# Performance work log

Measured on AMD Instinct MI355X. Metric: run time of the kernel, lower is better.

## Reference

```python
import jax, jax.numpy as jnp
import numpy as np

K = 20
CH_IN = [6, 128, 128, 256]
CH_OUT = [64, 64, 128, 256]
EMB = 1024


def _knn_idx(x, k):
    # x: (B, C, N) -> (B, N, k) indices of k nearest neighbors (incl. self)
    inner = jnp.einsum('bcn,bcm->bnm', x, x)
    xx = jnp.sum(x * x, axis=1)  # (B, N)
    pd = 2.0 * inner - xx[:, :, None] - xx[:, None, :]  # = -||xi - xj||^2
    return jax.lax.top_k(pd, k)[1]


def _graph_feature(x, k):
    # x: (B, C, N) -> (B, 2C, N, k) EdgeConv features [x_j - x_i, x_i]
    xt = jnp.transpose(x, (0, 2, 1))  # (B, N, C)
    idx = _knn_idx(x, k)  # (B, N, k)
    nb = jax.vmap(lambda f, i: f[i])(xt, idx)  # (B, N, k, C) gather
    center = xt[:, :, None, :]
    feat = jnp.concatenate([nb - center, jnp.broadcast_to(center, nb.shape)], axis=-1)
    return jnp.transpose(feat, (0, 3, 1, 2))  # (B, 2C, N, k)


def _bn(y, g, b, m, v):
    # eval-mode BatchNorm over channel axis 1 (or last for 2D input is also axis 1)
    shp = (1, -1) + (1,) * (y.ndim - 2)
    s = g / jnp.sqrt(v + 1e-5)
    return (y - m.reshape(shp)) * s.reshape(shp) + b.reshape(shp)


def setup_inputs() -> dict:
    key = jax.random.key(0)
    ks = iter(jax.random.split(key, 64))
    rn = lambda shape: jax.random.normal(next(ks), shape, jnp.float32) * 0.05
    ru = lambda shape: jax.random.uniform(next(ks), shape, jnp.float32, minval=0.5, maxval=1.5)
    d = {"x": jax.random.normal(next(ks), (16, 1024, 3), jnp.float32)}
    for i, (ci, co) in enumerate(zip(CH_IN, CH_OUT)):
        d[f"c{i}_w"] = rn((co, ci)); d[f"c{i}_b"] = rn((co,))
        d[f"c{i}_g"] = ru((co,)); d[f"c{i}_be"] = rn((co,))
        d[f"c{i}_m"] = rn((co,)); d[f"c{i}_v"] = ru((co,))
    cat = sum(CH_OUT)  # 512
    d["lc_w"] = rn((EMB, cat)); d["lc_b"] = rn((EMB,))
    d["lc_g"] = ru((EMB,)); d["lc_be"] = rn((EMB,))
    d["lc_m"] = rn((EMB,)); d["lc_v"] = ru((EMB,))
    d["l0_w"] = rn((512, 2 * EMB))
    d["l0_g"] = ru((512,)); d["l0_be"] = rn((512,)); d["l0_m"] = rn((512,)); d["l0_v"] = ru((512,))
    d["l1_w"] = rn((256, 512)); d["l1_b"] = rn((256,))
    d["l1_g"] = ru((256,)); d["l1_be"] = rn((256,)); d["l1_m"] = rn((256,)); d["l1_v"] = ru((256,))
    d["ow"] = rn((40, 256)); d["ob"] = rn((40,))
    return d


def reference(x, c0_w, c0_b, c0_g, c0_be, c0_m, c0_v,
              c1_w, c1_b, c1_g, c1_be, c1_m, c1_v,
              c2_w, c2_b, c2_g, c2_be, c2_m, c2_v,
              c3_w, c3_b, c3_g, c3_be, c3_m, c3_v,
              lc_w, lc_b, lc_g, lc_be, lc_m, lc_v,
              l0_w, l0_g, l0_be, l0_m, l0_v,
              l1_w, l1_b, l1_g, l1_be, l1_m, l1_v,
              ow, ob):
    convs = [(c0_w, c0_b, c0_g, c0_be, c0_m, c0_v),
             (c1_w, c1_b, c1_g, c1_be, c1_m, c1_v),
             (c2_w, c2_b, c2_g, c2_be, c2_m, c2_v),
             (c3_w, c3_b, c3_g, c3_be, c3_m, c3_v)]
    cur = jnp.transpose(x, (0, 2, 1))  # (B, 3, N)
    outs = []
    for w, b, g, be, m, v in convs:
        f = _graph_feature(cur, K)  # (B, 2C_in, N, k)
        y = jnp.einsum('bcnk,oc->bonk', f, w) + b[None, :, None, None]  # 1x1 conv2d
        y = jax.nn.leaky_relu(_bn(y, g, be, m, v), 0.2)
        cur = jnp.max(y, axis=-1)  # max over k neighbors -> (B, C_out, N)
        outs.append(cur)
    h = jnp.concatenate(outs, axis=1)  # (B, 512, N)
    y = jnp.einsum('bcn,oc->bon', h, lc_w) + lc_b[None, :, None]  # 1x1 conv1d
    y = jax.nn.leaky_relu(_bn(y, lc_g, lc_be, lc_m, lc_v), 0.2)  # (B, 1024, N)
    h = jnp.concatenate([jnp.max(y, axis=-1), jnp.mean(y, axis=-1)], axis=1)  # (B, 2048)
    h = jax.nn.leaky_relu(_bn(h @ l0_w.T, l0_g, l0_be, l0_m, l0_v), 0.2)
    h = jax.nn.leaky_relu(_bn(h @ l1_w.T + l1_b, l1_g, l1_be, l1_m, l1_v), 0.2)
    return h @ ow.T + ob  # (B, 40)
```

## Files before the change

### kernel.cpp

```cpp
#include <hip/hip_runtime.h>
#include <hip/hip_bf16.h>

#define BB 16
#define NPTS 1024
#define KNB 20
#define HC 512

__device__ __forceinline__ float XV(const float* __restrict__ X, int b, int n, int c)
{
    return X[((size_t)b * NPTS + n) * 3 + c];
}

__device__ __forceinline__ unsigned long long dist2key(float d, int m)
{
    unsigned u = __float_as_uint(d);
    u = (u & 0x80000000u) ? ~u : (u | 0x80000000u);
    return ((unsigned long long)u << 32) | (unsigned)(1023 - m);
}

__device__ __forceinline__ void wave_topk_write(unsigned long long* key,
                                                int* __restrict__ idxo,
                                                size_t obase, int lane)
{
    for (int it = 0; it < KNB; ++it) {
        unsigned long long best = 0ull; int bj = -1;
#pragma unroll
        for (int j = 0; j < 16; ++j) if (key[j] > best) { best = key[j]; bj = j; }
        unsigned long long wbest = best;
        for (int off = 32; off > 0; off >>= 1) {
            const unsigned long long o = __shfl_down(wbest, off, 64);
            if (o > wbest) wbest = o;
        }
        wbest = __shfl(wbest, 0, 64);
        if (best == wbest && bj >= 0) key[bj] = 0ull;
        if (lane == 0) idxo[obase + it] = 1023 - (int)(wbest & 0xFFFFFFFFull);
    }
}

__global__ void sentinel_kernel(float* __restrict__ out, float val)
{
    const int i = blockIdx.x * 256 + threadIdx.x;
    if (i < BB * 40) out[i] = val;
}

__global__ void xx_kernel(const float* __restrict__ H, const float* __restrict__ X,
                          float* __restrict__ xx, int cin, int off_in, int use_x)
{
    const int p = blockIdx.x * blockDim.x + threadIdx.x;
    if (p >= BB * NPTS) return;
    float s = 0.f;
    if (use_x) {
        const int b = p >> 10, n = p & 1023;
        for (int c = 0; c < 3; ++c) { const float v = XV(X, b, n, c); s += v * v; }
    } else {
        const float4* r4 = (const float4*)(H + (size_t)p * HC + off_in);
        for (int c4 = 0; c4 < cin / 4; ++c4) {
            const float4 v = r4[c4];
            s += v.x*v.x + v.y*v.y + v.z*v.z + v.w*v.w;
        }
    }
    xx[p] = s;
}

template<int CIN>
__global__ __launch_bounds__(256, 3) void knn4_kernel(
    const float* __restrict__ H, const float* __restrict__ xx,
    int* __restrict__ idxo, int off_in)
{
    __shared__ __align__(16) float qv[4][CIN];
    __shared__ float dist[4][NPTS];
    __shared__ float sxxq[4];
    const int blk = blockIdx.x;
    const int q0g = blk * 4;
    const int b = q0g >> 10, q0 = q0g & 1023;
    const int tid = threadIdx.x;
    const int base = b * NPTS;

    for (int t = tid; t < 4 * CIN; t += 256) {
        const int q = t / CIN, c = t - q * CIN;
        qv[q][c] = H[(size_t)(base + q0 + q) * HC + off_in + c];
    }
    if (tid < 4) sxxq[tid] = xx[base + q0 + tid];
    __syncthreads();

    const int g = tid >> 3, l = tid & 7;
    float4 aq[4][CIN / 32];
#pragma unroll
    for (int q = 0; q < 4; ++q)
#pragma unroll
        for (int r = 0; r < CIN / 32; ++r)
            aq[q][r] = *(const float4*)&qv[q][4 * (l + 8 * r)];

    for (int it = 0; it < 32; ++it) {
        const int m = g + 32 * it;
        float acc[4] = {0.f, 0.f, 0.f, 0.f};
#pragma unroll
        for (int r = 0; r < CIN / 32; ++r) {
            const float4 v = *(const float4*)(H + (size_t)(base + m) * HC + off_in + 4 * (l + 8 * r));
#pragma unroll
            for (int q = 0; q < 4; ++q)
                acc[q] += aq[q][r].x*v.x + aq[q][r].y*v.y + aq[q][r].z*v.z + aq[q][r].w*v.w;
        }
#pragma unroll
        for (int q = 0; q < 4; ++q) {
            acc[q] += __shfl_xor(acc[q], 1, 64);
            acc[q] += __shfl_xor(acc[q], 2, 64);
            acc[q] += __shfl_xor(acc[q], 4, 64);
        }
        if (l == 0) {
            const float xxm = xx[base + m];
#pragma unroll
            for (int q = 0; q < 4; ++q)
                dist[q][m] = (2.f * acc[q] - sxxq[q]) - xxm;
        }
    }
    __syncthreads();

    const int w = tid >> 6, lane = tid & 63;
    unsigned long long key[16];
#pragma unroll
    for (int j = 0; j < 16; ++j) {
        const int m = lane + 64 * j;
        key[j] = dist2key(dist[w][m], m);
    }
    wave_topk_write(key, idxo, (size_t)(base + q0 + w) * KNB, lane);
}

__global__ __launch_bounds__(256, 3) void knn4x_kernel(
    const float* __restrict__ X, const float* __restrict__ xx, int* __restrict__ idxo)
{
    __shared__ float qv[4][4];
    __shared__ float dist[4][NPTS];
    __shared__ float sxxq[4];
    const int blk = blockIdx.x;
    const int q0g = blk * 4;
    const int b = q0g >> 10, q0 = q0g & 1023;
    const int tid = threadIdx.x;
    const int base = b * NPTS;

    if (tid < 4) {
        for (int c = 0; c < 3; ++c) qv[tid][c] = XV(X, b, q0 + tid, c);
        sxxq[tid] = xx[base + q0 + tid];
    }
    __syncthreads();

    for (int j = 0; j < 4; ++j) {
        const int m = tid + 256 * j;
        const float r0 = XV(X, b, m, 0), r1 = XV(X, b, m, 1), r2 = XV(X, b, m, 2);
        const float xxm = xx[base + m];
#pragma unroll
        for (int q = 0; q < 4; ++q) {
            const float acc = qv[q][0]*r0 + qv[q][1]*r1 + qv[q][2]*r2;
            dist[q][m] = (2.f * acc - sxxq[q]) - xxm;
        }
    }
    __syncthreads();

    const int w = tid >> 6, lane = tid & 63;
    unsigned long long key[16];
#pragma unroll
    for (int j = 0; j < 16; ++j) {
        const int m = lane + 64 * j;
        key[j] = dist2key(dist[w][m], m);
    }
    wave_topk_write(key, idxo, (size_t)(base + q0 + w) * KNB, lane);
}

__device__ __forceinline__ float wfetch1(const float* __restrict__ W, int og,
                                         int CIN, int COUT, int c)
{
    if (og < COUT) return W[(size_t)og * 2 * CIN + c];
    const float* r0 = W + (size_t)(og - COUT) * 2 * CIN;
    return r0[CIN + c] - r0[c];
}

__global__ __launch_bounds__(256, 4) void gemm_conv_kernel(
    const float* __restrict__ H, const float* __restrict__ W, float* __restrict__ P,
    int off_in, int CIN, int COUT, int NO128)
{
    __shared__ float hl[32][68];
    __shared__ float wl[32][132];
    const int mblk = blockIdx.x / NO128;
    const int oblk = blockIdx.x - mblk * NO128;
    const int tid = threadIdx.x;
    const int o = tid & 63, grp = tid >> 6;
    const int NO = NO128 * 128;
    const int n0 = mblk * 64;
    const int og0 = oblk * 128 + o;
    const int og1 = og0 + 64;

    float acc0[16], acc1[16];
#pragma unroll
    for (int i = 0; i < 16; ++i) { acc0[i] = 0.f; acc1[i] = 0.f; }

    for (int ct = 0; ct < CIN / 32; ++ct) {
        for (int r = 0; r < 2; ++r) {
            const int e = tid + 256 * r;
            const int n = e & 63, c4 = e >> 6;
            const float4 hv = *(const float4*)(H + (size_t)(n0 + n) * HC + off_in + ct * 32 + c4 * 4);
            hl[c4*4+0][n] = hv.x; hl[c4*4+1][n] = hv.y; hl[c4*4+2][n] = hv.z; hl[c4*4+3][n] = hv.w;
        }
        for (int r = 0; r < 16; ++r) {
            const int e = tid + 256 * r;
            const int c_ = e & 31, o_ = e >> 5;
            wl[c_][o_] = wfetch1(W, oblk * 128 + o_, CIN, COUT, ct * 32 + c_);
        }
        __syncthreads();
        for (int c = 0; c < 32; ++c) {
            const float wva = wl[c][o];
            const float wvb = wl[c][o + 64];
            const float* hr = &hl[c][grp * 16];
#pragma unroll
            for (int nn = 0; nn < 4; ++nn) {
                const float4 hv = *(const float4*)(hr + 4 * nn);
                acc0[4*nn+0] += wva * hv.x; acc0[4*nn+1] += wva * hv.y;
                acc0[4*nn+2] += wva * hv.z; acc0[4*nn+3] += wva * hv.w;
                acc1[4*nn+0] += wvb * hv.x; acc1[4*nn+1] += wvb * hv.y;
                acc1[4*nn+2] += wvb * hv.z; acc1[4*nn+3] += wvb * hv.w;
            }
        }
        __syncthreads();
    }

#pragma unroll
    for (int i = 0; i < 16; ++i) {
        P[(size_t)(n0 + grp * 16 + i) * NO + og0] = acc0[i];
        P[(size_t)(n0 + grp * 16 + i) * NO + og1] = acc1[i];
    }
}

template<int COUT>
__global__ __launch_bounds__(COUT) void edge_epi_kernel(
    const float* __restrict__ P, const int* __restrict__ idx,
    const float* __restrict__ Bs, const float* __restrict__ G, const float* __restrict__ Be,
    const float* __restrict__ Bm, const float* __restrict__ Bv,
    float* __restrict__ Hout, int off_out)
{
    constexpr int NO = 2 * COUT;
    const int blk = blockIdx.x;
    const int base = (blk >> 10) << 10;
    const int o = threadIdx.x;
    const float s = G[o] / sqrtf(Bv[o] + 1e-5f);
    const float beo = Be[o];
    const float cb = P[(size_t)blk * NO + COUT + o] + Bs[o] - Bm[o];
    float mx = -INFINITY;
    for (int k = 0; k < KNB; ++k) {
        const int m = idx[(size_t)blk * KNB + k];
        const float v = P[(size_t)(base + m) * NO + o];
        float t = (v + cb) * s + beo;
        t = t > 0.f ? t : 0.2f * t;
        mx = fmaxf(mx, t);
    }
    Hout[(size_t)blk * HC + off_out + o] = mx;
}

template<int CIN, int COUT, bool USEX>
__global__ __launch_bounds__(COUT) void conv_kernel(
    const float* __restrict__ H, const float* __restrict__ X, const int* __restrict__ idx,
    const float* __restrict__ W, const float* __restrict__ Bs, const float* __restrict__ G,
    const float* __restrict__ Be, const float* __restrict__ Bm, const float* __restrict__ Bv,
    float* __restrict__ Hout, int off_in, int off_out)
{
    __shared__ __align__(16) float ctr[CIN];
    __shared__ __align__(16) float nb[KNB][CIN];
    __shared__ int sidx[KNB];
    const int blk = blockIdx.x;
    const int b = blk >> 10, q = blk & 1023;
    const int tid = threadIdx.x;
    const int base = b * NPTS;

    if (tid < KNB) sidx[tid] = idx[(size_t)(base + q) * KNB + tid];
    for (int c = tid; c < CIN; c += COUT)
        ctr[c] = USEX ? XV(X, b, q, c) : H[(size_t)(base + q) * HC + off_in + c];
    __syncthreads();
    for (int t = tid; t < KNB * CIN; t += COUT) {
        const int k = t / CIN, c = t - k * CIN;
        nb[k][c] = USEX ? XV(X, b, sidx[k], c) : H[(size_t)(base + sidx[k]) * HC + off_in + c];
    }
    __syncthreads();

    float acc[KNB];
    float cacc = 0.f;
#pragma unroll
    for (int k = 0; k < KNB; ++k) acc[k] = 0.f;

    const float* wr = W + (size_t)tid * 2 * CIN;
    for (int c = 0; c < CIN; ++c) {
        const float w1 = wr[c], w2 = wr[CIN + c];
        cacc += (w2 - w1) * ctr[c];
#pragma unroll
        for (int k = 0; k < KNB; ++k) acc[k] += w1 * nb[k][c];
    }

    const int o = tid;
    const float s = G[o] / sqrtf(Bv[o] + 1e-5f);
    const float beo = Be[o];
    const float cb = cacc + Bs[o] - Bm[o];
    float mx = -INFINITY;
#pragma unroll
    for (int k = 0; k < KNB; ++k) {
        float t = (acc[k] + cb) * s + beo;
        t = t > 0.f ? t : 0.2f * t;
        mx = fmaxf(mx, t);
    }
    Hout[(size_t)(base + q) * HC + off_out + o] = mx;
}

__global__ __launch_bounds__(256, 4) void lcpool_kernel(
    const float* __restrict__ H, const float* __restrict__ W, const float* __restrict__ Bs,
    const float* __restrict__ G, const float* __restrict__ Be,
    const float* __restrict__ Bm, const float* __restrict__ Bv,
    float* __restrict__ pmax, float* __restrict__ psum)
{
    __shared__ float hl[32][68];
    __shared__ float wl[32][132];
    __shared__ float redm[4][128];
    __shared__ float reds[4][128];
    const int bid = blockIdx.x;
    const int b = bid >> 7;
    const int rem = bid & 127;
    const int oblk = rem >> 4;
    const int nblk = rem & 15;
    const int tid = threadIdx.x;
    const int o = tid & 63;
    const int grp = tid >> 6;
    const int og0 = oblk * 128 + o;
    const int og1 = og0 + 64;
    const int n0 = nblk * 64;
    const size_t hbase = (size_t)b * NPTS * HC;

    float acc0[16], acc1[16];
#pragma unroll
    for (int i = 0; i < 16; ++i) { acc0[i] = 0.f; acc1[i] = 0.f; }

    for (int ct = 0; ct < 16; ++ct) {
        for (int r = 0; r < 2; ++r) {
            const int e = tid + 256 * r;
            const int n = e & 63, c4 = e >> 6;
            const float4 hv = *(const float4*)(H + hbase + (size_t)(n0 + n) * HC + ct * 32 + c4 * 4);
            hl[c4*4+0][n] = hv.x; hl[c4*4+1][n] = hv.y; hl[c4*4+2][n] = hv.z; hl[c4*4+3][n] = hv.w;
        }
        for (int r = 0; r < 16; ++r) {
            const int e = tid + 256 * r;
            const int c_ = e & 31, o_ = e >> 5;
            wl[c_][o_] = W[(size_t)(oblk * 128 + o_) * HC + ct * 32 + c_];
        }
        __syncthreads();
        for (int c = 0; c < 32; ++c) {
            const float wva = wl[c][o];
            const float wvb = wl[c][o + 64];
            const float* hr = &hl[c][grp * 16];
#pragma unroll
            for (int nn = 0; nn < 4; ++nn) {
                const float4 hv = *(const float4*)(hr + 4 * nn);
                acc0[4*nn+0] += wva * hv.x; acc0[4*nn+1] += wva * hv.y;
                acc0[4*nn+2] += wva * hv.z; acc0[4*nn+3] += wva * hv.w;
                acc1[4*nn+0] += wvb * hv.x; acc1[4*nn+1] += wvb * hv.y;
                acc1[4*nn+2] += wvb * hv.z; acc1[4*nn+3] += wvb * hv.w;
            }
        }
        __syncthreads();
    }

#pragma unroll
    for (int p = 0; p < 2; ++p) {
        const int og = p ? og1 : og0;
        const float* acc = p ? acc1 : acc0;
        const float s = G[og] / sqrtf(Bv[og] + 1e-5f);
        const float beo = Be[og];
        const float mb = Bs[og] - Bm[og];
        float pm = -INFINITY, ps = 0.f;
#pragma unroll
        for (int i = 0; i < 16; ++i) {
            float t = (acc[i] + mb) * s + beo;
            t = t > 0.f ? t : 0.2f * t;
            pm = fmaxf(pm, t); ps += t;
        }
        redm[grp][o + 64 * p] = pm; reds[grp][o + 64 * p] = ps;
    }
    __syncthreads();
    if (grp == 0) {
#pragma unroll
        for (int p = 0; p < 2; ++p) {
            const int oo = o + 64 * p;
            float m0 = redm[0][oo], s0 = reds[0][oo];
            for (int i2 = 1; i2 < 4; ++i2) { m0 = fmaxf(m0, redm[i2][oo]); s0 += reds[i2][oo]; }
            pmax[((size_t)b * 16 + nblk) * 1024 + oblk * 128 + oo] = m0;
            psum[((size_t)b * 16 + nblk) * 1024 + oblk * 128 + oo] = s0;
        }
    }
}

__global__ void pool_reduce_kernel(const float* __restrict__ pmax, const float* __restrict__ psum,
                                   float* __restrict__ h2)
{
    const int i = blockIdx.x * 256 + threadIdx.x;
    if (i >= BB * 1024) return;
    const int b = i >> 10, o = i & 1023;
    float mx = -INFINITY, sm = 0.f;
    for (int c = 0; c < 16; ++c) {
        mx = fmaxf(mx, pmax[((size_t)b * 16 + c) * 1024 + o]);
        sm += psum[((size_t)b * 16 + c) * 1024 + o];
    }
    h2[(size_t)b * 2048 + o] = mx;
    h2[(size_t)b * 2048 + 1024 + o] = sm * (1.f / 1024.f);
}

__global__ void l0_kernel(const float* __restrict__ h2, const float* __restrict__ W,
                          const float* __restrict__ G, const float* __restrict__ Be,
                          const float* __restrict__ Bm, const float* __restrict__ Bv,
                          float* __restrict__ h3)
{
    const int i = blockIdx.x * 256 + threadIdx.x;
    if (i >= BB * 512) return;
    const int b = i >> 9, o = i & 511;
    const float4* w4 = (const float4*)(W + (size_t)o * 2048);
    const float4* h4p = (const float4*)(h2 + (size_t)b * 2048);
    float acc = 0.f;
    for (int c = 0; c < 512; ++c) {
        const float4 wv = w4[c]; const float4 hv = h4p[c];
        acc += wv.x*hv.x + wv.y*hv.y + wv.z*hv.z + wv.w*hv.w;
    }
    const float s = G[o] / sqrtf(Bv[o] + 1e-5f);
    float t = (acc - Bm[o]) * s + Be[o];
    t = t > 0.f ? t : 0.2f * t;
    h3[(size_t)b * 512 + o] = t;
}

__global__ void l1_kernel(const float* __restrict__ h3, const float* __restrict__ W,
                          const float* __restrict__ Bs, const float* __restrict__ G,
                          const float* __restrict__ Be, const float* __restrict__ Bm,
                          const float* __restrict__ Bv, float* __restrict__ h4o)
{
    const int i = blockIdx.x * 256 + threadIdx.x;
    if (i >= BB * 256) return;
    const int b = i >> 8, o = i & 255;
    const float4* w4 = (const float4*)(W + (size_t)o * 512);
    const float4* hv4 = (const float4*)(h3 + (size_t)b * 512);
    float acc = 0.f;
    for (int c = 0; c < 128; ++c) {
        const float4 wv = w4[c]; const float4 hv = hv4[c];
        acc += wv.x*hv.x + wv.y*hv.y + wv.z*hv.z + wv.w*hv.w;
    }
    acc += Bs[o];
    const float s = G[o] / sqrtf(Bv[o] + 1e-5f);
    float t = (acc - Bm[o]) * s + Be[o];
    t = t > 0.f ? t : 0.2f * t;
    h4o[(size_t)b * 256 + o] = t;
}

__global__ void out_kernel(const float* __restrict__ h4, const float* __restrict__ W,
                           const float* __restrict__ Bs, float* __restrict__ out)
{
    const int i = blockIdx.x * 256 + threadIdx.x;
    if (i >= BB * 40) return;
    const int b = i / 40, o = i % 40;
    const float4* w4 = (const float4*)(W + (size_t)o * 256);
    const float4* hv4 = (const float4*)(h4 + (size_t)b * 256);
    float acc = 0.f;
    for (int c = 0; c < 64; ++c) {
        const float4 wv = w4[c]; const float4 hv = hv4[c];
        acc += wv.x*hv.x + wv.y*hv.y + wv.z*hv.z + wv.w*hv.w;
    }
    acc += Bs[o];
    out[(size_t)b * 40 + o] = acc;
}

extern "C" void kernel_launch(void* const* d_in, const int* in_sizes, int n_in,
                              void* d_out, int out_size, void* d_ws, size_t ws_size,
                              hipStream_t stream)
{
    static const int expect[44] = {
        49152, 384,64,64,64,64,64, 8192,64,64,64,64,64, 16384,128,128,128,128,128,
        65536,256,256,256,256,256, 524288,1024,1024,1024,1024,1024,
        1048576,512,512,512,512, 131072,256,256,256,256,256, 10240,40};
    int bad = -1;
    if (n_in != 44) bad = 100;
    else if (out_size != BB * 40) bad = 101;
    else {
        for (int i = 0; i < 44; ++i) if (in_sizes[i] != expect[i]) { bad = i; break; }
    }
    if (bad >= 0) {
        sentinel_kernel<<<3, 256, 0, stream>>>((float*)d_out, 500.f + (float)bad);
        return;
    }

    const float* X = (const float*)d_in[0];
    const float *CW[4], *CB[4], *CG[4], *CBE[4], *CM[4], *CV[4];
    for (int i = 0; i < 4; ++i) {
        CW[i]  = (const float*)d_in[1 + 6*i]; CB[i] = (const float*)d_in[2 + 6*i];
        CG[i]  = (const float*)d_in[3 + 6*i]; CBE[i] = (const float*)d_in[4 + 6*i];
        CM[i]  = (const float*)d_in[5 + 6*i]; CV[i] = (const float*)d_in[6 + 6*i];
    }
    const float* LCW = (const float*)d_in[25]; const float* LCB = (const float*)d_in[26];
    const float* LCG = (const float*)d_in[27]; const float* LCBE = (const float*)d_in[28];
    const float* LCM = (const float*)d_in[29]; const float* LCV = (const float*)d_in[30];
    const float* L0W = (const float*)d_in[31]; const float* L0G = (const float*)d_in[32];
    const float* L0BE = (const float*)d_in[33]; const float* L0M = (const float*)d_in[34];
    const float* L0V = (const float*)d_in[35];
    const float* L1W = (const float*)d_in[36]; const float* L1B = (const float*)d_in[37];
    const float* L1G = (const float*)d_in[38]; const float* L1BE = (const float*)d_in[39];
    const float* L1M = (const float*)d_in[40]; const float* L1V = (const float*)d_in[41];
    const float* OW = (const float*)d_in[42]; const float* OB = (const float*)d_in[43];

    float* H    = (float*)d_ws;
    float* XX   = H + (size_t)BB * NPTS * HC;
    int*   IDX  = (int*)(XX + BB * NPTS);
    float* P    = (float*)(IDX + (size_t)BB * NPTS * KNB);
    float* PMAX = P + (size_t)BB * NPTS * 512;
    float* PSUM = PMAX + BB * 16 * 1024;
    float* H2   = PSUM + BB * 16 * 1024;
    float* H3   = H2 + BB * 2048;
    float* H4   = H3 + BB * 512;
    const size_t need_bytes = (size_t)((H4 + BB * 256) - H) * 4;
    const bool use_P = (ws_size >= need_bytes);

    float* fPMAX = P;
    float* fPSUM = fPMAX + BB * 16 * 1024;
    float* fH2   = fPSUM + BB * 16 * 1024;
    float* fH3   = fH2 + BB * 2048;
    float* fH4   = fH3 + BB * 512;

    const int M = BB * NPTS;

    xx_kernel<<<M/256, 256, 0, stream>>>(H, X, XX, 3, 0, 1);
    knn4x_kernel<<<M/4, 256, 0, stream>>>(X, XX, IDX);
    conv_kernel<3,64,true><<<M, 64, 0, stream>>>(H, X, IDX,
        CW[0], CB[0], CG[0], CBE[0], CM[0], CV[0], H, 0, 0);

    if (use_P) {
        xx_kernel<<<M/256, 256, 0, stream>>>(H, X, XX, 64, 0, 0);
        knn4_kernel<64><<<M/4, 256, 0, stream>>>(H, XX, IDX, 0);
        gemm_conv_kernel<<<(M/64)*1, 256, 0, stream>>>(H, CW[1], P, 0, 64, 64, 1);
        edge_epi_kernel<64><<<M, 64, 0, stream>>>(P, IDX,
            CB[1], CG[1], CBE[1], CM[1], CV[1], H, 64);

        xx_kernel<<<M/256, 256, 0, stream>>>(H, X, XX, 64, 64, 0);
        knn4_kernel<64><<<M/4, 256, 0, stream>>>(H, XX, IDX, 64);
        gemm_conv_kernel<<<(M/64)*2, 256, 0, stream>>>(H, CW[2], P, 64, 64, 128, 2);
        edge_epi_kernel<128><<<M, 128, 0, stream>>>(P, IDX,
            CB[2], CG[2], CBE[2], CM[2], CV[2], H, 128);

        xx_kernel<<<M/256, 256, 0, stream>>>(H, X, XX, 128, 128, 0);
        knn4_kernel<128><<<M/4, 256, 0, stream>>>(H, XX, IDX, 128);
        gemm_conv_kernel<<<(M/64)*4, 256, 0, stream>>>(H, CW[3], P, 128, 128, 256, 4);
        edge_epi_kernel<256><<<M, 256, 0, stream>>>(P, IDX,
            CB[3], CG[3], CBE[3], CM[3], CV[3], H, 256);

        lcpool_kernel<<<BB*8*16, 256, 0, stream>>>(H, LCW, LCB, LCG, LCBE, LCM, LCV, PMAX, PSUM);
        pool_reduce_kernel<<<BB*1024/256, 256, 0, stream>>>(PMAX, PSUM, H2);
        l0_kernel<<<(BB*512+255)/256, 256, 0, stream>>>(H2, L0W, L0G, L0BE, L0M, L0V, H3);
        l1_kernel<<<(BB*256+255)/256, 256, 0, stream>>>(H3, L1W, L1B, L1G, L1BE, L1M, L1V, H4);
        out_kernel<<<(BB*40+255)/256, 256, 0, stream>>>(H4, OW, OB, (float*)d_out);
    } else {
        xx_kernel<<<M/256, 256, 0, stream>>>(H, X, XX, 64, 0, 0);
        knn4_kernel<64><<<M/4, 256, 0, stream>>>(H, XX, IDX, 0);
        conv_kernel<64,64,false><<<M, 64, 0, stream>>>(H, X, IDX,
            CW[1], CB[1], CG[1], CBE[1], CM[1], CV[1], H, 0, 64);

        xx_kernel<<<M/256, 256, 0, stream>>>(H, X, XX, 64, 64, 0);
        knn4_kernel<64><<<M/4, 256, 0, stream>>>(H, XX, IDX, 64);
        conv_kernel<64,128,false><<<M, 128, 0, stream>>>(H, X, IDX,
            CW[2], CB[2], CG[2], CBE[2], CM[2], CV[2], H, 64, 128);

        xx_kernel<<<M/256, 256, 0, stream>>>(H, X, XX, 128, 128, 0);
        knn4_kernel<128><<<M/4, 256, 0, stream>>>(H, XX, IDX, 128);
        conv_kernel<128,256,false><<<M, 256, 0, stream>>>(H, X, IDX,
            CW[3], CB[3], CG[3], CBE[3], CM[3], CV[3], H, 128, 256);

        lcpool_kernel<<<BB*8*16, 256, 0, stream>>>(H, LCW, LCB, LCG, LCBE, LCM, LCV, fPMAX, fPSUM);
        pool_reduce_kernel<<<BB*1024/256, 256, 0, stream>>>(fPMAX, fPSUM, fH2);
        l0_kernel<<<(BB*512+255)/256, 256, 0, stream>>>(fH2, L0W, L0G, L0BE, L0M, L0V, fH3);
        l1_kernel<<<(BB*256+255)/256, 256, 0, stream>>>(fH3, L1W, L1B, L1G, L1BE, L1M, L1V, fH4);
        out_kernel<<<(BB*40+255)/256, 256, 0, stream>>>(fH4, OW, OB, (float*)d_out);
    }
}
```

Baseline: 1.248 ms.

## Process eight kNN queries per block for 64-channel layers and pad GEMM LDS tiles

Adds a knn8 kernel for the 64-channel EdgeConv layers. Each block computes distances for eight query points, so every candidate feature row loaded from global memory is reused across eight queries instead of four. Eight lanes split the channel dot product with register-held query vectors and combine it with shuffles, and each wave then runs top-k over two queries. Separately, the weight shared-memory tile in the GEMM and lcpool kernels is padded from 132 to 133 columns to change the bank-conflict pattern. The trade-offs are twice the distance shared memory per block (lower occupancy), more serial top-k work per wave, and a padded stride that breaks 16-byte alignment of the tile rows.

```diff
diff --git a/kernel.cpp b/kernel.cpp
--- a/kernel.cpp
+++ b/kernel.cpp
@@ -62,6 +62,72 @@
     xx[p] = s;
 }
 
+__global__ __launch_bounds__(256, 3) void knn8_kernel(
+    const float* __restrict__ H, const float* __restrict__ xx,
+    int* __restrict__ idxo, int off_in)
+{
+    constexpr int CIN = 64;
+    __shared__ __align__(16) float qv[8][CIN];
+    __shared__ float dist[8][NPTS];
+    __shared__ float sxxq[8];
+    const int blk = blockIdx.x;
+    const int q0g = blk * 8;
+    const int b = q0g >> 10, q0 = q0g & 1023;
+    const int tid = threadIdx.x;
+    const int base = b * NPTS;
+
+    for (int t = tid; t < 8 * CIN; t += 256) {
+        const int q = t >> 6, c = t & 63;
+        qv[q][c] = H[(size_t)(base + q0 + q) * HC + off_in + c];
+    }
+    if (tid < 8) sxxq[tid] = xx[base + q0 + tid];
+    __syncthreads();
+
+    const int g = tid >> 3, l = tid & 7;
+    float4 aq[8][2];
+#pragma unroll
+    for (int q = 0; q < 8; ++q)
+#pragma unroll
+        for (int r = 0; r < 2; ++r)
+            aq[q][r] = *(const float4*)&qv[q][4 * (l + 8 * r)];
+
+    for (int it = 0; it < 32; ++it) {
+        const int m = g + 32 * it;
+        float acc[8] = {0.f,0.f,0.f,0.f,0.f,0.f,0.f,0.f};
+#pragma unroll
+        for (int r = 0; r < 2; ++r) {
+            const float4 v = *(const float4*)(H + (size_t)(base + m) * HC + off_in + 4 * (l + 8 * r));
+#pragma unroll
+            for (int q = 0; q < 8; ++q)
+                acc[q] += aq[q][r].x*v.x + aq[q][r].y*v.y + aq[q][r].z*v.z + aq[q][r].w*v.w;
+        }
+#pragma unroll
+        for (int q = 0; q < 8; ++q) {
+            acc[q] += __shfl_xor(acc[q], 1, 64);
+            acc[q] += __shfl_xor(acc[q], 2, 64);
+            acc[q] += __shfl_xor(acc[q], 4, 64);
+        }
+        if (l == 0) {
+            const float xxm = xx[base + m];
+#pragma unroll
+            for (int q = 0; q < 8; ++q)
+                dist[q][m] = (2.f * acc[q] - sxxq[q]) - xxm;
+        }
+    }
+    __syncthreads();
+
+    const int w = tid >> 6, lane = tid & 63;
+    for (int qq = w; qq < 8; qq += 4) {
+        unsigned long long key[16];
+#pragma unroll
+        for (int j = 0; j < 16; ++j) {
+            const int m = lane + 64 * j;
+            key[j] = dist2key(dist[qq][m], m);
+        }
+        wave_topk_write(key, idxo, (size_t)(base + q0 + qq) * KNB, lane);
+    }
+}
+
 template<int CIN>
 __global__ __launch_bounds__(256, 3) void knn4_kernel(
     const float* __restrict__ H, const float* __restrict__ xx,
@@ -179,7 +245,7 @@
     int off_in, int CIN, int COUT, int NO128)
 {
     __shared__ float hl[32][68];
-    __shared__ float wl[32][132];
+    __shared__ float wl[32][133];
     const int mblk = blockIdx.x / NO128;
     const int oblk = blockIdx.x - mblk * NO128;
     const int tid = threadIdx.x;
@@ -313,7 +379,7 @@
     float* __restrict__ pmax, float* __restrict__ psum)
 {
     __shared__ float hl[32][68];
-    __shared__ float wl[32][132];
+    __shared__ float wl[32][133];
     __shared__ float redm[4][128];
     __shared__ float reds[4][128];
     const int bid = blockIdx.x;
@@ -530,13 +596,13 @@
 
     if (use_P) {
         xx_kernel<<<M/256, 256, 0, stream>>>(H, X, XX, 64, 0, 0);
-        knn4_kernel<64><<<M/4, 256, 0, stream>>>(H, XX, IDX, 0);
+        knn8_kernel<<<M/8, 256, 0, stream>>>(H, XX, IDX, 0);
         gemm_conv_kernel<<<(M/64)*1, 256, 0, stream>>>(H, CW[1], P, 0, 64, 64, 1);
         edge_epi_kernel<64><<<M, 64, 0, stream>>>(P, IDX,
             CB[1], CG[1], CBE[1], CM[1], CV[1], H, 64);
 
         xx_kernel<<<M/256, 256, 0, stream>>>(H, X, XX, 64, 64, 0);
-        knn4_kernel<64><<<M/4, 256, 0, stream>>>(H, XX, IDX, 64);
+        knn8_kernel<<<M/8, 256, 0, stream>>>(H, XX, IDX, 64);
         gemm_conv_kernel<<<(M/64)*2, 256, 0, stream>>>(H, CW[2], P, 64, 64, 128, 2);
         edge_epi_kernel<128><<<M, 128, 0, stream>>>(P, IDX,
             CB[2], CG[2], CBE[2], CM[2], CV[2], H, 128);
@@ -554,12 +620,12 @@
         out_kernel<<<(BB*40+255)/256, 256, 0, stream>>>(H4, OW, OB, (float*)d_out);
     } else {
         xx_kernel<<<M/256, 256, 0, stream>>>(H, X, XX, 64, 0, 0);
-        knn4_kernel<64><<<M/4, 256, 0, stream>>>(H, XX, IDX, 0);
+        knn8_kernel<<<M/8, 256, 0, stream>>>(H, XX, IDX, 0);
         conv_kernel<64,64,false><<<M, 64, 0, stream>>>(H, X, IDX,
             CW[1], CB[1], CG[1], CBE[1], CM[1], CV[1], H, 0, 64);
 
         xx_kernel<<<M/256, 256, 0, stream>>>(H, X, XX, 64, 64, 0);
-        knn4_kernel<64><<<M/4, 256, 0, stream>>>(H, XX, IDX, 64);
+        knn8_kernel<<<M/8, 256, 0, stream>>>(H, XX, IDX, 64);
         conv_kernel<64,128,false><<<M, 128, 0, stream>>>(H, X, IDX,
             CW[2], CB[2], CG[2], CBE[2], CM[2], CV[2], H, 64, 128);
 
```

After: 1.264 ms. Within noise of the previous version (+1.3%).
